# Optimization experiments

Hardware: AMD Instinct MI355X
Metric: run time of the kernel (lower is better)

## Reference

```python
import jax, jax.numpy as jnp
import numpy as np

EMBED_DIM = 256
NUM_HEADS = 8
NUM_LEVELS = 4
NUM_POINTS = 4
HEAD_DIM = EMBED_DIM // NUM_HEADS


def _bilinear_sample(img, x, y):
    """img: [N,C,H,W]; x,y: [N,P] absolute pixel coords (align_corners=False mapping
    already applied by caller). Zero padding outside, matching F.grid_sample."""
    N, C, H, W = img.shape
    x0 = jnp.floor(x)
    y0 = jnp.floor(y)
    wx1 = x - x0
    wy1 = y - y0
    img_flat = img.reshape(N, C, H * W)

    def gather(ix, iy):
        valid = ((ix >= 0) & (ix <= W - 1) & (iy >= 0) & (iy <= H - 1)).astype(img.dtype)
        idx = (jnp.clip(iy, 0, H - 1) * W + jnp.clip(ix, 0, W - 1)).astype(jnp.int32)
        v = jnp.take_along_axis(img_flat, idx[:, None, :], axis=2)  # [N,C,P]
        return v * valid[:, None, :]

    return (gather(x0, y0) * ((1.0 - wx1) * (1.0 - wy1))[:, None, :]
            + gather(x0 + 1.0, y0) * (wx1 * (1.0 - wy1))[:, None, :]
            + gather(x0, y0 + 1.0) * ((1.0 - wx1) * wy1)[:, None, :]
            + gather(x0 + 1.0, y0 + 1.0) * (wx1 * wy1)[:, None, :])


def _reference_points(H, W):
    yy, xx = jnp.meshgrid(jnp.arange(H, dtype=jnp.float32), jnp.arange(W, dtype=jnp.float32), indexing='ij')
    # stack order is (x, y), matching grid_sample's (x=width, y=height) convention
    return jnp.stack([(xx + 0.5) / W, (yy + 0.5) / H], axis=-1).reshape(H * W, 2)


def _frame_attention(q_feat, values, level_shapes, Wq, bq, Woff, boff, Wattn, battn, Wout, bout):
    Bt, C, H, W = q_feat.shape
    N = H * W
    q = q_feat.reshape(Bt, C, N).transpose(0, 2, 1) @ Wq + bq  # [Bt,N,C]
    off = (q @ Woff + boff).reshape(Bt, N, NUM_HEADS, NUM_LEVELS, NUM_POINTS, 2)
    aw = jax.nn.softmax((q @ Wattn + battn).reshape(Bt, N, NUM_HEADS, NUM_LEVELS * NUM_POINTS), axis=-1)
    aw = aw.reshape(Bt, N, NUM_HEADS, NUM_LEVELS, NUM_POINTS)
    ref = _reference_points(H, W)  # [N,2]
    sampled = []
    for l, (val, (Hl, Wl)) in enumerate(zip(values, level_shapes)):
        loc = ref[None, :, None, None, :] + off[:, :, :, l] / jnp.array([Wl, Hl], dtype=q.dtype)
        grid = jnp.clip(loc, 0.0, 1.0) * 2.0 - 1.0  # [Bt,N,M,K,2]
        grid = grid.transpose(0, 2, 1, 3, 4).reshape(Bt * NUM_HEADS, N * NUM_POINTS, 2)
        # align_corners=False: pixel = ((g+1)*size - 1)/2
        x = ((grid[..., 0] + 1.0) * Wl - 1.0) * 0.5
        y = ((grid[..., 1] + 1.0) * Hl - 1.0) * 0.5
        s = _bilinear_sample(val, x, y)  # [Bt*M, hd, N*K]
        s = s.reshape(Bt, NUM_HEADS, HEAD_DIM, N, NUM_POINTS).transpose(0, 3, 1, 4, 2)  # [Bt,N,M,K,hd]
        sampled.append(s)
    samp = jnp.stack(sampled, axis=3)  # [Bt,N,M,L,K,hd]
    out = (samp * aw[..., None]).sum(axis=(3, 4)).reshape(Bt, N, C)
    out = out @ Wout + bout
    return out.transpose(0, 2, 1).reshape(Bt, C, H, W)


def _forward(feats, Wq, bq, Wv, bv, Woff, boff, Wattn, battn, Wout, bout):
    B, C, H0, W0, T = feats[0].shape
    # original loops over frames t; frames are independent, so fold T into batch
    feats_bt = [jnp.moveaxis(f, -1, 1).reshape(f.shape[0] * T, C, f.shape[2], f.shape[3]) for f in feats]
    level_shapes = [(f.shape[2], f.shape[3]) for f in feats_bt]
    Bt = B * T
    # value projection per level (identical across query scales; compute once)
    values = []
    for f, (Hl, Wl) in zip(feats_bt, level_shapes):
        v = f.reshape(Bt, C, Hl * Wl).transpose(0, 2, 1) @ Wv + bv  # [Bt,HW,C]
        v = v.reshape(Bt, Hl * Wl, NUM_HEADS, HEAD_DIM).transpose(0, 2, 3, 1).reshape(Bt * NUM_HEADS, HEAD_DIM, Hl, Wl)
        values.append(v)
    outs = []
    for f, (Hl, Wl) in zip(feats_bt, level_shapes):
        o = _frame_attention(f, values, level_shapes, Wq, bq, Woff, boff, Wattn, battn, Wout, bout)
        outs.append(o.reshape(B, T, C, Hl, Wl).transpose(0, 2, 3, 4, 1))  # back to [B,C,H,W,T]
    return tuple(outs)


def setup_inputs() -> dict:
    key = jax.random.key(0)
    ks = jax.random.split(key, 10)
    B, T, C = 2, 2, EMBED_DIM
    shapes = [(64, 64), (32, 32), (16, 16), (8, 8)]
    inp = {}
    for i, (H, W) in enumerate(shapes):
        inp[f"feats{i}"] = jax.random.normal(ks[i], (B, C, H, W, T), dtype=jnp.float32)
    s = float(1.0 / np.sqrt(C))
    noff = NUM_HEADS * NUM_LEVELS * NUM_POINTS
    inp["Wq"] = jax.random.normal(ks[4], (C, C), jnp.float32) * s
    inp["bq"] = jnp.zeros((C,), jnp.float32)
    inp["Wv"] = jax.random.normal(ks[5], (C, C), jnp.float32) * s
    inp["bv"] = jnp.zeros((C,), jnp.float32)
    inp["Woff"] = jax.random.normal(ks[6], (C, noff * 2), jnp.float32) * 0.01
    inp["boff"] = jax.random.normal(ks[7], (noff * 2,), jnp.float32) * 2.0
    inp["Wattn"] = jax.random.normal(ks[8], (C, noff), jnp.float32) * 0.01
    inp["battn"] = jnp.zeros((noff,), jnp.float32)
    inp["Wout"] = jax.random.normal(ks[9], (C, C), jnp.float32) * s
    inp["bout"] = jnp.zeros((C,), jnp.float32)
    return inp


def reference(feats0, feats1, feats2, feats3, Wq, bq, Wv, bv, Woff, boff, Wattn, battn, Wout, bout):
    return _forward([feats0, feats1, feats2, feats3], Wq, bq, Wv, bv, Woff, boff, Wattn, battn, Wout, bout)
```

## Files before the change

kernel.cpp:

```cpp
#include <hip/hip_runtime.h>
#include <hip/hip_bf16.h>

#define NR 21760

typedef short short8 __attribute__((ext_vector_type(8)));
typedef float f32x4 __attribute__((ext_vector_type(4)));

__device__ __forceinline__ int level_of_row(int R) {
    if (R < 16384) return 0;
    if (R < 20480) return 1;
    if (R < 21504) return 2;
    return 3;
}

__device__ __forceinline__ unsigned pk2(float a, float b) {
    __hip_bfloat16 x = __float2bfloat16(a), y = __float2bfloat16(b);
    return (unsigned)*(unsigned short*)&x | ((unsigned)*(unsigned short*)&y << 16);
}

__global__ __launch_bounds__(256) void pack_all_kernel(const float* __restrict__ f0,
                                                       const float* __restrict__ f1,
                                                       const float* __restrict__ f2,
                                                       const float* __restrict__ f3,
                                                       __hip_bfloat16* __restrict__ XP) {
    int bx = blockIdx.x;
    const float* f; int nj, Wl, rowbase, rel;
    if (bx < 1024)      { f = f0; nj = 128; Wl = 64; rowbase = 0;     rel = bx; }
    else if (bx < 1280) { f = f1; nj = 32;  Wl = 32; rowbase = 16384; rel = bx - 1024; }
    else if (bx < 1344) { f = f2; nj = 8;   Wl = 16; rowbase = 20480; rel = bx - 1280; }
    else                { f = f3; nj = 2;   Wl = 8;  rowbase = 21504; rel = bx - 1344; }
    const int HW = Wl * Wl;
    const int HWT = HW * 2;
    const int j0 = (rel % nj) * 64;
    const int c0 = ((rel / nj) & 3) * 64;
    const int b  = rel / (nj * 4);
    const int tid = threadIdx.x;
    __shared__ float tile[64][65];
    {
        const int cl = tid >> 2, q = tid & 3;
        const float* fb = f + (size_t)(b * 256 + c0 + cl) * HWT + j0 + q * 16;
#pragma unroll
        for (int k = 0; k < 4; ++k) {
            float4 v = *(const float4*)(fb + k * 4);
            *(float4*)(&tile[cl][q * 16 + k * 4]) = v;
        }
    }
    __syncthreads();
    {
        const int jl = tid >> 4, cq = tid & 15;
#pragma unroll
        for (int pass = 0; pass < 4; ++pass) {
            int jloc = pass * 16 + jl;
            int j = j0 + jloc;
            int p = j >> 1, t = j & 1;
            int row = rowbase + (b * 2 + t) * HW + p;
            float v0 = tile[cq * 4 + 0][jloc];
            float v1 = tile[cq * 4 + 1][jloc];
            float v2 = tile[cq * 4 + 2][jloc];
            float v3 = tile[cq * 4 + 3][jloc];
            uint2 o;
            o.x = pk2(v0, v1); o.y = pk2(v2, v3);
            *(uint2*)(&XP[(size_t)row * 256 + c0 + cq * 4]) = o;
        }
    }
}

__global__ __launch_bounds__(256) void wtrans_all_kernel(const float* __restrict__ Wq,
                                                         const float* __restrict__ Wv,
                                                         const float* __restrict__ Woff,
                                                         const float* __restrict__ Wattn,
                                                         const float* __restrict__ Wout,
                                                         const float* __restrict__ bq,
                                                         const float* __restrict__ boff,
                                                         const float* __restrict__ battn,
                                                         __hip_bfloat16* __restrict__ WTvo,
                                                         __hip_bfloat16* __restrict__ WTout,
                                                         float* __restrict__ bias_oa) {
    const int bx = blockIdx.x;
    const int tid = threadIdx.x;
    if (bx == 224) {
        {
            int n = tid;
            float s = 0.f;
            for (int j = 0; j < 256; ++j) s += bq[j] * Woff[(size_t)j * 256 + n];
            bias_oa[n] = s + boff[n];
        }
        if (tid < 128) {
            int n = tid;
            float s = 0.f;
            for (int j = 0; j < 256; ++j) s += bq[j] * Wattn[(size_t)j * 128 + n];
            bias_oa[256 + n] = s + battn[n];
        }
        return;
    }
    if (bx >= 128) {
        const int rel = bx - 128;
        const int n0 = (rel % 12) * 32, k0 = (rel / 12) * 32;
        const int n = tid & 31, kt = tid >> 5;
        const int nn = n0 + n;
        float acc[4] = {0.f, 0.f, 0.f, 0.f};
        for (int j = 0; j < 256; ++j) {
            float wo = (nn < 256) ? Woff[(size_t)j * 256 + nn]
                                  : Wattn[(size_t)j * 128 + nn - 256];
#pragma unroll
            for (int i = 0; i < 4; ++i)
                acc[i] += wo * Wq[(size_t)(k0 + kt * 4 + i) * 256 + j];
        }
#pragma unroll
        for (int i = 0; i < 4; ++i)
            WTvo[(size_t)(256 + nn) * 256 + k0 + kt * 4 + i] = __float2bfloat16(acc[i]);
        return;
    }
    __shared__ float t[32][33];
    const float* W = (bx < 64) ? Wv : Wout;
    __hip_bfloat16* WT = (bx < 64) ? WTvo : WTout;
    const int rel = bx & 63;
    const int n0 = (rel % 8) * 32, k0 = (rel / 8) * 32;
    const int c = tid & 31, r = tid >> 5;
#pragma unroll
    for (int i = 0; i < 4; ++i)
        t[r + 8 * i][c] = W[(size_t)(k0 + r + 8 * i) * 256 + n0 + c];
    __syncthreads();
#pragma unroll
    for (int i = 0; i < 4; ++i)
        WT[(size_t)(n0 + r + 8 * i) * 256 + k0 + c] = __float2bfloat16(t[c][r + 8 * i]);
}

__global__ __launch_bounds__(256) void gemm64_dual(const __hip_bfloat16* __restrict__ A,
                                                   const __hip_bfloat16* __restrict__ BT,
                                                   const float* __restrict__ bias,
                                                   const float* __restrict__ bias2,
                                                   __hip_bfloat16* __restrict__ VAL,
                                                   float* __restrict__ OA) {
    __shared__ __align__(16) __hip_bfloat16 As[64][72];
    __shared__ __align__(16) __hip_bfloat16 Bs[64][72];
    const int m0 = blockIdx.x * 64;
    const int n0 = blockIdx.y * 64;
    const int w = threadIdx.x >> 6;
    const int lane = threadIdx.x & 63;
    const int wm = (w >> 1) * 32;
    const int wn = (w & 1) * 32;
    const int fr = lane & 15;
    const int fq = lane >> 4;
    const int srow = threadIdx.x >> 3;
    const int schunk = threadIdx.x & 7;
    f32x4 acc[2][2] = {};

    for (int kt = 0; kt < 256; kt += 64) {
        __syncthreads();
#pragma unroll
        for (int i = 0; i < 2; ++i) {
            int r = srow + 32 * i;
            float4 va = *(const float4*)(&A[(size_t)(m0 + r) * 256 + kt + schunk * 8]);
            *(float4*)(&As[r][schunk * 8]) = va;
            float4 vb = *(const float4*)(&BT[(size_t)(n0 + r) * 256 + kt + schunk * 8]);
            *(float4*)(&Bs[r][schunk * 8]) = vb;
        }
        __syncthreads();
#pragma unroll
        for (int ks = 0; ks < 2; ++ks) {
            short8 a[2], b[2];
#pragma unroll
            for (int fi = 0; fi < 2; ++fi)
                a[fi] = *(const short8*)(&As[wm + fi * 16 + fr][ks * 32 + fq * 8]);
#pragma unroll
            for (int fj = 0; fj < 2; ++fj)
                b[fj] = *(const short8*)(&Bs[wn + fj * 16 + fr][ks * 32 + fq * 8]);
#pragma unroll
            for (int fi = 0; fi < 2; ++fi)
#pragma unroll
                for (int fj = 0; fj < 2; ++fj)
                    acc[fi][fj] = __builtin_amdgcn_mfma_f32_16x16x32_bf16(
                        a[fi], b[fj], acc[fi][fj], 0, 0, 0);
        }
    }

    if (n0 < 256) {
#pragma unroll
        for (int fi = 0; fi < 2; ++fi)
#pragma unroll
            for (int fj = 0; fj < 2; ++fj) {
                int col = n0 + wn + fj * 16 + fr;
                float bb = bias[col];
#pragma unroll
                for (int r = 0; r < 4; ++r) {
                    int row = m0 + wm + fi * 16 + fq * 4 + r;
                    VAL[(size_t)row * 256 + col] = __float2bfloat16(acc[fi][fj][r] + bb);
                }
            }
    } else {
#pragma unroll
        for (int fi = 0; fi < 2; ++fi)
#pragma unroll
            for (int fj = 0; fj < 2; ++fj) {
                int c2 = n0 - 256 + wn + fj * 16 + fr;
                float bb = bias2[c2];
#pragma unroll
                for (int r = 0; r < 4; ++r) {
                    int row = m0 + wm + fi * 16 + fq * 4 + r;
                    OA[(size_t)row * 384 + c2] = acc[fi][fj][r] + bb;
                }
            }
    }
}

__global__ __launch_bounds__(256) void gemm_scatter_kernel(const __hip_bfloat16* __restrict__ A,
                                                           const __hip_bfloat16* __restrict__ BT,
                                                           const float* __restrict__ bias,
                                                           float* __restrict__ out) {
    const int bx = blockIdx.x;
    int l, b, p0;
    if (bx < 256)      { l = 0; b = bx >> 7;          p0 = (bx & 127) * 32; }
    else if (bx < 320) { l = 1; b = (bx - 256) >> 5;  p0 = ((bx - 256) & 31) * 32; }
    else if (bx < 336) { l = 2; b = (bx - 320) >> 3;  p0 = ((bx - 320) & 7) * 32; }
    else               { l = 3; b = (bx - 336) >> 1;  p0 = ((bx - 336) & 1) * 32; }
    const int qbase[4]    = {0, 16384, 20480, 21504};
    const int hwtab[4]    = {4096, 1024, 256, 64};
    const size_t obase[4] = {0, 4194304, 5242880, 5505024};
    const int HW = hwtab[l];
    const int qb = qbase[l];

    __shared__ __align__(16) __hip_bfloat16 As[64][72];
    __shared__ __align__(16) __hip_bfloat16 Bs[64][72];
    const int n0 = blockIdx.y * 64;
    const int w = threadIdx.x >> 6;
    const int lane = threadIdx.x & 63;
    const int wm = (w >> 1) * 32;
    const int wn = (w & 1) * 32;
    const int fr = lane & 15;
    const int fq = lane >> 4;
    const int srow = threadIdx.x >> 3;
    const int schunk = threadIdx.x & 7;
    f32x4 acc[2][2] = {};

    for (int kt = 0; kt < 256; kt += 64) {
        __syncthreads();
#pragma unroll
        for (int i = 0; i < 2; ++i) {
            int m = srow + 32 * i;
            int t = (m >> 4) & 1;
            int pl = (m & 15) | ((m & 32) >> 1);
            int R = qb + (2 * b + t) * HW + p0 + pl;
            float4 va = *(const float4*)(&A[(size_t)R * 256 + kt + schunk * 8]);
            *(float4*)(&As[m][schunk * 8]) = va;
            float4 vb = *(const float4*)(&BT[(size_t)(n0 + m) * 256 + kt + schunk * 8]);
            *(float4*)(&Bs[m][schunk * 8]) = vb;
        }
        __syncthreads();
#pragma unroll
        for (int ks = 0; ks < 2; ++ks) {
            short8 a[2], bfr[2];
#pragma unroll
            for (int fi = 0; fi < 2; ++fi)
                a[fi] = *(const short8*)(&As[wm + fi * 16 + fr][ks * 32 + fq * 8]);
#pragma unroll
            for (int fj = 0; fj < 2; ++fj)
                bfr[fj] = *(const short8*)(&Bs[wn + fj * 16 + fr][ks * 32 + fq * 8]);
#pragma unroll
            for (int fi = 0; fi < 2; ++fi)
#pragma unroll
                for (int fj = 0; fj < 2; ++fj)
                    acc[fi][fj] = __builtin_amdgcn_mfma_f32_16x16x32_bf16(
                        a[fi], bfr[fj], acc[fi][fj], 0, 0, 0);
        }
    }
    const int plbase = fq * 4 + ((wm & 32) >> 1);
#pragma unroll
    for (int fj = 0; fj < 2; ++fj) {
        int col = n0 + wn + fj * 16 + fr;
        float bb = bias[col];
#pragma unroll
        for (int r = 0; r < 4; ++r) {
            int p = p0 + plbase + r;
            size_t addr = obase[l] + (((size_t)b * 256 + col) * HW + p) * 2;
            float2 v;
            v.x = acc[0][fj][r] + bb;
            v.y = acc[1][fj][r] + bb;
            *(float2*)(out + addr) = v;
        }
    }
}

__device__ __forceinline__ void acc8(f32x4& a, f32x4& b, uint4 v, float w) {
    a[0] = fmaf(w, __uint_as_float(v.x << 16),          a[0]);
    a[1] = fmaf(w, __uint_as_float(v.x & 0xffff0000u),  a[1]);
    a[2] = fmaf(w, __uint_as_float(v.y << 16),          a[2]);
    a[3] = fmaf(w, __uint_as_float(v.y & 0xffff0000u),  a[3]);
    b[0] = fmaf(w, __uint_as_float(v.z << 16),          b[0]);
    b[1] = fmaf(w, __uint_as_float(v.z & 0xffff0000u),  b[1]);
    b[2] = fmaf(w, __uint_as_float(v.w << 16),          b[2]);
    b[3] = fmaf(w, __uint_as_float(v.w & 0xffff0000u),  b[3]);
}

#define QB 4
__global__ __launch_bounds__(256, 2) void sample_kernel(const __hip_bfloat16* __restrict__ VAL,
                                                        const float* __restrict__ OA,
                                                        __hip_bfloat16* __restrict__ SAMP) {
    __shared__ __align__(16) int2 tapd[QB * 512];
    const int R0 = blockIdx.x * QB;
    const int tid = threadIdx.x;
    const int qbase[4] = {0, 16384, 20480, 21504};
    const int wsh[4]   = {6, 5, 4, 3};
    const int hwsh[4]  = {12, 10, 8, 6};
    const float invwf[4] = {1.f/64.f, 1.f/32.f, 1.f/16.f, 1.f/8.f};

    if (tid < QB * 32) {
        const int qh = tid >> 2, part = tid & 3;
        const int q = qh >> 3, h = qh & 7;
        const int R = R0 + q;
        const int lq = level_of_row(R);
        const int r2 = R - qbase[lq];
        const int bt = r2 >> hwsh[lq];
        const int p  = r2 & ((1 << hwsh[lq]) - 1);
        const int pxi = p & ((1 << wsh[lq]) - 1);
        const int pyi = p >> wsh[lq];
        const float refx = (pxi + 0.5f) * invwf[lq];
        const float refy = (pyi + 0.5f) * invwf[lq];
        const float* oarow = OA + (size_t)R * 384;
        float4 offA = *(const float4*)(oarow + h * 32 + part * 8);
        float4 offB = *(const float4*)(oarow + h * 32 + part * 8 + 4);
        float4 awv  = *(const float4*)(oarow + 256 + h * 16 + part * 4);
        float m = fmaxf(fmaxf(awv.x, awv.y), fmaxf(awv.z, awv.w));
        m = fmaxf(m, __shfl_xor(m, 1));
        m = fmaxf(m, __shfl_xor(m, 2));
        float e0 = __expf(awv.x - m), e1 = __expf(awv.y - m);
        float e2 = __expf(awv.z - m), e3 = __expf(awv.w - m);
        float s = e0 + e1 + e2 + e3;
        s += __shfl_xor(s, 1);
        s += __shfl_xor(s, 2);
        const float inv = 1.0f / s;
        const int l = part;
        const int Wl = 1 << wsh[l];
        const float invWf = invwf[l];
        const int base = (qbase[l] + (bt << hwsh[l])) << 8;
        float oxy[8] = {offA.x, offA.y, offA.z, offA.w, offB.x, offB.y, offB.z, offB.w};
        float ee[4] = {e0, e1, e2, e3};
#pragma unroll
        for (int i = 0; i < 4; ++i) {
            float ox = oxy[2 * i], oy = oxy[2 * i + 1];
            float aw = ee[i] * inv;
            float lx = fminf(fmaxf(refx + ox * invWf, 0.f), 1.f);
            float ly = fminf(fmaxf(refy + oy * invWf, 0.f), 1.f);
            float px = lx * Wl - 0.5f;
            float py = ly * Wl - 0.5f;
            float x0f = floorf(px), y0f = floorf(py);
            int x0 = (int)x0f, y0 = (int)y0f;
            float wx = px - x0f, wy = py - y0f;
            float vx0 = (x0 >= 0) ? 1.f : 0.f;
            float vx1 = (x0 + 1 <= Wl - 1) ? 1.f : 0.f;
            float vy0 = (y0 >= 0) ? 1.f : 0.f;
            float vy1 = (y0 + 1 <= Wl - 1) ? 1.f : 0.f;
            int x0c = max(x0, 0), x1c = min(x0 + 1, Wl - 1);
            int y0c = max(y0, 0), y1c = min(y0 + 1, Wl - 1);
            int o00 = base + (((y0c << wsh[l]) + x0c) << 8);
            int o10 = base + (((y0c << wsh[l]) + x1c) << 8);
            int o01 = base + (((y1c << wsh[l]) + x0c) << 8);
            int o11 = base + (((y1c << wsh[l]) + x1c) << 8);
            float w00 = aw * (1.f - wx) * (1.f - wy) * vx0 * vy0;
            float w10 = aw * wx * (1.f - wy) * vx1 * vy0;
            float w01 = aw * (1.f - wx) * wy * vx0 * vy1;
            float w11 = aw * wx * wy * vx1 * vy1;
            int idx = ((q * 16 + part * 4 + i) * 8 + h) * 4;
            *(int4*)(&tapd[idx])     = make_int4(o00, __float_as_int(w00), o10, __float_as_int(w10));
            *(int4*)(&tapd[idx + 2]) = make_int4(o01, __float_as_int(w01), o11, __float_as_int(w11));
        }
    }
    __syncthreads();

    const int wq = tid >> 6, lane = tid & 63;
    const int u = lane >> 2, sub = lane & 3;
    const int c = u & 3, h4 = u >> 2;
    const int R = R0 + wq;
    const __hip_bfloat16* v0base = VAL + h4 * 32 + sub * 8;
    const __hip_bfloat16* v1base = VAL + (h4 + 4) * 32 + sub * 8;
    const int2* tp = &tapd[wq * 512];
    f32x4 aA0 = {0,0,0,0}, aA1 = {0,0,0,0};
    f32x4 aB0 = {0,0,0,0}, aB1 = {0,0,0,0};
#pragma unroll 2
    for (int t = 0; t < 16; ++t) {
        int2 d0 = tp[(t * 8 + h4) * 4 + c];
        int2 d1 = tp[(t * 8 + h4 + 4) * 4 + c];
        uint4 x0 = *(const uint4*)(v0base + d0.x);
        uint4 x1 = *(const uint4*)(v1base + d1.x);
        acc8(aA0, aA1, x0, __int_as_float(d0.y));
        acc8(aB0, aB1, x1, __int_as_float(d1.y));
    }
#pragma unroll
    for (int i = 0; i < 4; ++i) {
        aA0[i] += __shfl_xor(aA0[i], 4); aA0[i] += __shfl_xor(aA0[i], 8);
        aA1[i] += __shfl_xor(aA1[i], 4); aA1[i] += __shfl_xor(aA1[i], 8);
        aB0[i] += __shfl_xor(aB0[i], 4); aB0[i] += __shfl_xor(aB0[i], 8);
        aB1[i] += __shfl_xor(aB1[i], 4); aB1[i] += __shfl_xor(aB1[i], 8);
    }
    if (c == 0) {
        uint4 o0, o1;
        o0.x = pk2(aA0[0], aA0[1]); o0.y = pk2(aA0[2], aA0[3]);
        o0.z = pk2(aA1[0], aA1[1]); o0.w = pk2(aA1[2], aA1[3]);
        o1.x = pk2(aB0[0], aB0[1]); o1.y = pk2(aB0[2], aB0[3]);
        o1.z = pk2(aB1[0], aB1[1]); o1.w = pk2(aB1[2], aB1[3]);
        *(uint4*)(&SAMP[(size_t)R * 256 + h4 * 32 + sub * 8]) = o0;
        *(uint4*)(&SAMP[(size_t)R * 256 + (h4 + 4) * 32 + sub * 8]) = o1;
    }
}

extern "C" void kernel_launch(void* const* d_in, const int* in_sizes, int n_in,
                              void* d_out, int out_size, void* d_ws, size_t ws_size,
                              hipStream_t stream) {
    (void)in_sizes; (void)n_in; (void)out_size; (void)ws_size;
    const float* f0 = (const float*)d_in[0];
    const float* f1 = (const float*)d_in[1];
    const float* f2 = (const float*)d_in[2];
    const float* f3 = (const float*)d_in[3];
    const float* Wq    = (const float*)d_in[4];
    const float* bq    = (const float*)d_in[5];
    const float* Wv    = (const float*)d_in[6];
    const float* bv    = (const float*)d_in[7];
    const float* Woff  = (const float*)d_in[8];
    const float* boff  = (const float*)d_in[9];
    const float* Wattn = (const float*)d_in[10];
    const float* battn = (const float*)d_in[11];
    const float* Wout  = (const float*)d_in[12];
    const float* bout  = (const float*)d_in[13];
    float* out = (float*)d_out;

    char* w = (char*)d_ws;
    __hip_bfloat16* XPb   = (__hip_bfloat16*)w;   w += (size_t)NR * 256 * 2;
    __hip_bfloat16* SAMPb = (__hip_bfloat16*)w;   w += (size_t)NR * 256 * 2;
    __hip_bfloat16* VAL   = (__hip_bfloat16*)w;   w += (size_t)NR * 256 * 2;
    float* OA   = (float*)w;                      w += (size_t)NR * 384 * 4;
    __hip_bfloat16* WTvo  = (__hip_bfloat16*)w;   w += 640 * 256 * 2;
    __hip_bfloat16* WTout = (__hip_bfloat16*)w;   w += 256 * 256 * 2;
    float* bias_oa = (float*)w;                   w += 384 * 4;

    hipLaunchKernelGGL(pack_all_kernel, dim3(1360), dim3(256), 0, stream, f0, f1, f2, f3, XPb);

    hipLaunchKernelGGL(wtrans_all_kernel, dim3(225), dim3(256), 0, stream,
                       Wq, Wv, Woff, Wattn, Wout, bq, boff, battn,
                       WTvo, WTout, bias_oa);

    hipLaunchKernelGGL(gemm64_dual, dim3(NR / 64, 10), dim3(256), 0, stream,
                       XPb, WTvo, bv, bias_oa, VAL, OA);

    hipLaunchKernelGGL(sample_kernel, dim3(NR / QB), dim3(256), 0, stream, VAL, OA, SAMPb);

    hipLaunchKernelGGL(gemm_scatter_kernel, dim3(340, 4), dim3(256), 0, stream,
                       SAMPb, WTout, bout, out);
}
```

Before: 105.4 us.

## Merge pack and weight-transform kernels; enlarge projection GEMM tile to 128x64

```diff
diff --git a/kernel.cpp b/kernel.cpp
--- a/kernel.cpp
+++ b/kernel.cpp
@@ -18,87 +18,90 @@
     return (unsigned)*(unsigned short*)&x | ((unsigned)*(unsigned short*)&y << 16);
 }
 
-__global__ __launch_bounds__(256) void pack_all_kernel(const float* __restrict__ f0,
-                                                       const float* __restrict__ f1,
-                                                       const float* __restrict__ f2,
-                                                       const float* __restrict__ f3,
-                                                       __hip_bfloat16* __restrict__ XP) {
-    int bx = blockIdx.x;
-    const float* f; int nj, Wl, rowbase, rel;
-    if (bx < 1024)      { f = f0; nj = 128; Wl = 64; rowbase = 0;     rel = bx; }
-    else if (bx < 1280) { f = f1; nj = 32;  Wl = 32; rowbase = 16384; rel = bx - 1024; }
-    else if (bx < 1344) { f = f2; nj = 8;   Wl = 16; rowbase = 20480; rel = bx - 1280; }
-    else                { f = f3; nj = 2;   Wl = 8;  rowbase = 21504; rel = bx - 1344; }
-    const int HW = Wl * Wl;
-    const int HWT = HW * 2;
-    const int j0 = (rel % nj) * 64;
-    const int c0 = ((rel / nj) & 3) * 64;
-    const int b  = rel / (nj * 4);
+__global__ __launch_bounds__(256) void prep_kernel(const float* __restrict__ f0,
+                                                   const float* __restrict__ f1,
+                                                   const float* __restrict__ f2,
+                                                   const float* __restrict__ f3,
+                                                   const float* __restrict__ Wq,
+                                                   const float* __restrict__ Wv,
+                                                   const float* __restrict__ Woff,
+                                                   const float* __restrict__ Wattn,
+                                                   const float* __restrict__ Wout,
+                                                   const float* __restrict__ bq,
+                                                   const float* __restrict__ boff,
+                                                   const float* __restrict__ battn,
+                                                   __hip_bfloat16* __restrict__ XP,
+                                                   __hip_bfloat16* __restrict__ WTvo,
+                                                   __hip_bfloat16* __restrict__ WTout,
+                                                   float* __restrict__ bias_oa) {
+    const int bx = blockIdx.x;
     const int tid = threadIdx.x;
     __shared__ float tile[64][65];
-    {
-        const int cl = tid >> 2, q = tid & 3;
-        const float* fb = f + (size_t)(b * 256 + c0 + cl) * HWT + j0 + q * 16;
-#pragma unroll
-        for (int k = 0; k < 4; ++k) {
-            float4 v = *(const float4*)(fb + k * 4);
-            *(float4*)(&tile[cl][q * 16 + k * 4]) = v;
-        }
-    }
-    __syncthreads();
-    {
-        const int jl = tid >> 4, cq = tid & 15;
-#pragma unroll
-        for (int pass = 0; pass < 4; ++pass) {
-            int jloc = pass * 16 + jl;
-            int j = j0 + jloc;
-            int p = j >> 1, t = j & 1;
-            int row = rowbase + (b * 2 + t) * HW + p;
-            float v0 = tile[cq * 4 + 0][jloc];
-            float v1 = tile[cq * 4 + 1][jloc];
-            float v2 = tile[cq * 4 + 2][jloc];
-            float v3 = tile[cq * 4 + 3][jloc];
-            uint2 o;
-            o.x = pk2(v0, v1); o.y = pk2(v2, v3);
-            *(uint2*)(&XP[(size_t)row * 256 + c0 + cq * 4]) = o;
-        }
-    }
-}
-
-__global__ __launch_bounds__(256) void wtrans_all_kernel(const float* __restrict__ Wq,
-                                                         const float* __restrict__ Wv,
-                                                         const float* __restrict__ Woff,
-                                                         const float* __restrict__ Wattn,
-                                                         const float* __restrict__ Wout,
-                                                         const float* __restrict__ bq,
-                                                         const float* __restrict__ boff,
-                                                         const float* __restrict__ battn,
-                                                         __hip_bfloat16* __restrict__ WTvo,
-                                                         __hip_bfloat16* __restrict__ WTout,
-                                                         float* __restrict__ bias_oa) {
-    const int bx = blockIdx.x;
-    const int tid = threadIdx.x;
-    if (bx == 224) {
+
+    if (bx < 1360) {
+        const float* f; int nj, Wl, rowbase, rel;
+        if (bx < 1024)      { f = f0; nj = 128; Wl = 64; rowbase = 0;     rel = bx; }
+        else if (bx < 1280) { f = f1; nj = 32;  Wl = 32; rowbase = 16384; rel = bx - 1024; }
+        else if (bx < 1344) { f = f2; nj = 8;   Wl = 16; rowbase = 20480; rel = bx - 1280; }
+        else                { f = f3; nj = 2;   Wl = 8;  rowbase = 21504; rel = bx - 1344; }
+        const int HW = Wl * Wl;
+        const int HWT = HW * 2;
+        const int j0 = (rel % nj) * 64;
+        const int c0 = ((rel / nj) & 3) * 64;
+        const int b  = rel / (nj * 4);
+        {
+            const int cl = tid >> 2, q = tid & 3;
+            const float* fb = f + (size_t)(b * 256 + c0 + cl) * HWT + j0 + q * 16;
+#pragma unroll
+            for (int k = 0; k < 4; ++k) {
+                float4 v = *(const float4*)(fb + k * 4);
+                *(float4*)(&tile[cl][q * 16 + k * 4]) = v;
+            }
+        }
+        __syncthreads();
+        {
+            const int jl = tid >> 4, cq = tid & 15;
+#pragma unroll
+            for (int pass = 0; pass < 4; ++pass) {
+                int jloc = pass * 16 + jl;
+                int j = j0 + jloc;
+                int p = j >> 1, t = j & 1;
+                int row = rowbase + (b * 2 + t) * HW + p;
+                float v0 = tile[cq * 4 + 0][jloc];
+                float v1 = tile[cq * 4 + 1][jloc];
+                float v2 = tile[cq * 4 + 2][jloc];
+                float v3 = tile[cq * 4 + 3][jloc];
+                uint2 o;
+                o.x = pk2(v0, v1); o.y = pk2(v2, v3);
+                *(uint2*)(&XP[(size_t)row * 256 + c0 + cq * 4]) = o;
+            }
+        }
+        return;
+    }
+    if (bx == 1584) {
         {
             int n = tid;
             float s = 0.f;
+#pragma unroll 8
             for (int j = 0; j < 256; ++j) s += bq[j] * Woff[(size_t)j * 256 + n];
             bias_oa[n] = s + boff[n];
         }
         if (tid < 128) {
             int n = tid;
             float s = 0.f;
+#pragma unroll 8
             for (int j = 0; j < 256; ++j) s += bq[j] * Wattn[(size_t)j * 128 + n];
             bias_oa[256 + n] = s + battn[n];
         }
         return;
     }
-    if (bx >= 128) {
-        const int rel = bx - 128;
+    if (bx >= 1488) {
+        const int rel = bx - 1488;
         const int n0 = (rel % 12) * 32, k0 = (rel / 12) * 32;
         const int n = tid & 31, kt = tid >> 5;
         const int nn = n0 + n;
         float acc[4] = {0.f, 0.f, 0.f, 0.f};
+#pragma unroll 8
         for (int j = 0; j < 256; ++j) {
             float wo = (nn < 256) ? Woff[(size_t)j * 256 + nn]
                                   : Wattn[(size_t)j * 128 + nn - 256];
@@ -111,65 +114,66 @@
             WTvo[(size_t)(256 + nn) * 256 + k0 + kt * 4 + i] = __float2bfloat16(acc[i]);
         return;
     }
-    __shared__ float t[32][33];
-    const float* W = (bx < 64) ? Wv : Wout;
-    __hip_bfloat16* WT = (bx < 64) ? WTvo : WTout;
-    const int rel = bx & 63;
+    const float* W = (bx < 1424) ? Wv : Wout;
+    __hip_bfloat16* WT = (bx < 1424) ? WTvo : WTout;
+    const int rel = (bx - 1360) & 63;
     const int n0 = (rel % 8) * 32, k0 = (rel / 8) * 32;
     const int c = tid & 31, r = tid >> 5;
 #pragma unroll
     for (int i = 0; i < 4; ++i)
-        t[r + 8 * i][c] = W[(size_t)(k0 + r + 8 * i) * 256 + n0 + c];
+        tile[r + 8 * i][c] = W[(size_t)(k0 + r + 8 * i) * 256 + n0 + c];
     __syncthreads();
 #pragma unroll
     for (int i = 0; i < 4; ++i)
-        WT[(size_t)(n0 + r + 8 * i) * 256 + k0 + c] = __float2bfloat16(t[c][r + 8 * i]);
-}
-
-__global__ __launch_bounds__(256) void gemm64_dual(const __hip_bfloat16* __restrict__ A,
-                                                   const __hip_bfloat16* __restrict__ BT,
-                                                   const float* __restrict__ bias,
-                                                   const float* __restrict__ bias2,
-                                                   __hip_bfloat16* __restrict__ VAL,
-                                                   float* __restrict__ OA) {
-    __shared__ __align__(16) __hip_bfloat16 As[64][72];
+        WT[(size_t)(n0 + r + 8 * i) * 256 + k0 + c] = __float2bfloat16(tile[c][r + 8 * i]);
+}
+
+__global__ __launch_bounds__(256) void gemm12864_dual(const __hip_bfloat16* __restrict__ A,
+                                                      const __hip_bfloat16* __restrict__ BT,
+                                                      const float* __restrict__ bias,
+                                                      const float* __restrict__ bias2,
+                                                      __hip_bfloat16* __restrict__ VAL,
+                                                      float* __restrict__ OA) {
+    __shared__ __align__(16) __hip_bfloat16 As[128][72];
     __shared__ __align__(16) __hip_bfloat16 Bs[64][72];
-    const int m0 = blockIdx.x * 64;
+    const int m0 = blockIdx.x * 128;
     const int n0 = blockIdx.y * 64;
     const int w = threadIdx.x >> 6;
     const int lane = threadIdx.x & 63;
-    const int wm = (w >> 1) * 32;
-    const int wn = (w & 1) * 32;
     const int fr = lane & 15;
     const int fq = lane >> 4;
     const int srow = threadIdx.x >> 3;
     const int schunk = threadIdx.x & 7;
-    f32x4 acc[2][2] = {};
+    f32x4 acc[2][4] = {};
 
     for (int kt = 0; kt < 256; kt += 64) {
         __syncthreads();
 #pragma unroll
-        for (int i = 0; i < 2; ++i) {
+        for (int i = 0; i < 4; ++i) {
             int r = srow + 32 * i;
             float4 va = *(const float4*)(&A[(size_t)(m0 + r) * 256 + kt + schunk * 8]);
             *(float4*)(&As[r][schunk * 8]) = va;
+        }
+#pragma unroll
+        for (int i = 0; i < 2; ++i) {
+            int r = srow + 32 * i;
             float4 vb = *(const float4*)(&BT[(size_t)(n0 + r) * 256 + kt + schunk * 8]);
             *(float4*)(&Bs[r][schunk * 8]) = vb;
         }
         __syncthreads();
 #pragma unroll
         for (int ks = 0; ks < 2; ++ks) {
-            short8 a[2], b[2];
-#pragma unroll
-            for (int fi = 0; fi < 2; ++fi)
-                a[fi] = *(const short8*)(&As[wm + fi * 16 + fr][ks * 32 + fq * 8]);
-#pragma unroll
-            for (int fj = 0; fj < 2; ++fj)
-                b[fj] = *(const short8*)(&Bs[wn + fj * 16 + fr][ks * 32 + fq * 8]);
-#pragma unroll
-            for (int fi = 0; fi < 2; ++fi)
-#pragma unroll
-                for (int fj = 0; fj < 2; ++fj)
+            short8 a[2], b[4];
+#pragma unroll
+            for (int fi = 0; fi < 2; ++fi)
+                a[fi] = *(const short8*)(&As[w * 32 + fi * 16 + fr][ks * 32 + fq * 8]);
+#pragma unroll
+            for (int fj = 0; fj < 4; ++fj)
+                b[fj] = *(const short8*)(&Bs[fj * 16 + fr][ks * 32 + fq * 8]);
+#pragma unroll
+            for (int fi = 0; fi < 2; ++fi)
+#pragma unroll
+                for (int fj = 0; fj < 4; ++fj)
                     acc[fi][fj] = __builtin_amdgcn_mfma_f32_16x16x32_bf16(
                         a[fi], b[fj], acc[fi][fj], 0, 0, 0);
         }
@@ -177,30 +181,30 @@
 
     if (n0 < 256) {
 #pragma unroll
-        for (int fi = 0; fi < 2; ++fi)
-#pragma unroll
-            for (int fj = 0; fj < 2; ++fj) {
-                int col = n0 + wn + fj * 16 + fr;
-                float bb = bias[col];
+        for (int fj = 0; fj < 4; ++fj) {
+            int col = n0 + fj * 16 + fr;
+            float bb = bias[col];
+#pragma unroll
+            for (int fi = 0; fi < 2; ++fi)
 #pragma unroll
                 for (int r = 0; r < 4; ++r) {
-                    int row = m0 + wm + fi * 16 + fq * 4 + r;
+                    int row = m0 + w * 32 + fi * 16 + fq * 4 + r;
                     VAL[(size_t)row * 256 + col] = __float2bfloat16(acc[fi][fj][r] + bb);
                 }
-            }
+        }
     } else {
 #pragma unroll
-        for (int fi = 0; fi < 2; ++fi)
-#pragma unroll
-            for (int fj = 0; fj < 2; ++fj) {
-                int c2 = n0 - 256 + wn + fj * 16 + fr;
-                float bb = bias2[c2];
+        for (int fj = 0; fj < 4; ++fj) {
+            int c2 = n0 - 256 + fj * 16 + fr;
+            float bb = bias2[c2];
+#pragma unroll
+            for (int fi = 0; fi < 2; ++fi)
 #pragma unroll
                 for (int r = 0; r < 4; ++r) {
-                    int row = m0 + wm + fi * 16 + fq * 4 + r;
+                    int row = m0 + w * 32 + fi * 16 + fq * 4 + r;
                     OA[(size_t)row * 384 + c2] = acc[fi][fj][r] + bb;
                 }
-            }
+        }
     }
 }
 
@@ -432,13 +436,11 @@
     __hip_bfloat16* WTout = (__hip_bfloat16*)w;   w += 256 * 256 * 2;
     float* bias_oa = (float*)w;                   w += 384 * 4;
 
-    hipLaunchKernelGGL(pack_all_kernel, dim3(1360), dim3(256), 0, stream, f0, f1, f2, f3, XPb);
-
-    hipLaunchKernelGGL(wtrans_all_kernel, dim3(225), dim3(256), 0, stream,
-                       Wq, Wv, Woff, Wattn, Wout, bq, boff, battn,
-                       WTvo, WTout, bias_oa);
-
-    hipLaunchKernelGGL(gemm64_dual, dim3(NR / 64, 10), dim3(256), 0, stream,
+    hipLaunchKernelGGL(prep_kernel, dim3(1585), dim3(256), 0, stream,
+                       f0, f1, f2, f3, Wq, Wv, Woff, Wattn, Wout, bq, boff, battn,
+                       XPb, WTvo, WTout, bias_oa);
+
+    hipLaunchKernelGGL(gemm12864_dual, dim3(NR / 128, 10), dim3(256), 0, stream,
                        XPb, WTvo, bv, bias_oa, VAL, OA);
 
     hipLaunchKernelGGL(sample_kernel, dim3(NR / QB), dim3(256), 0, stream, VAL, OA, SAMPb);
```

After: 104.2 us. Within noise of the previous version (-1.1%).
